# Kernel tuning notes

Measured on AMD Instinct MI355X. Metric: run time of the kernel, lower is better.

The kernel has to match this reference:

```python
import jax, jax.numpy as jnp
import numpy as np

B, L, C, K = 32, 8192, 32, 5  # batch, positions, channels(=filters), kernel_size
F = C  # residual add requires filters == input channels
BN_EPS = 1e-3      # keras BatchNormalization default epsilon
LEAKY_ALPHA = 0.3  # keras LeakyReLU default alpha


def setup_inputs() -> dict:
    key = jax.random.key(0)
    ks = jax.random.split(key, 4)
    # RandomUniform(-limit, limit) with limit = sqrt(2*3 / (2*K*F**2))
    limit = float(np.sqrt(2.0 * 3.0 / (2.0 * K * F * F)))
    return {
        "x": jax.random.normal(ks[0], (B, L, C), dtype=jnp.float32),
        # LocallyConnected 1: K unshared kernels [L, C, F], bias [L, F]
        "k1": jax.random.uniform(ks[1], (K, L, C, F), minval=-limit, maxval=limit, dtype=jnp.float32),
        "b1": jnp.zeros((L, F), dtype=jnp.float32),
        "gamma1": jnp.ones((F,), dtype=jnp.float32),
        "beta1": jnp.zeros((F,), dtype=jnp.float32),
        "mean1": jnp.zeros((F,), dtype=jnp.float32),
        "var1": jnp.ones((F,), dtype=jnp.float32),
        # LocallyConnected 2
        "k2": jax.random.uniform(ks[2], (K, L, F, F), minval=-limit, maxval=limit, dtype=jnp.float32),
        "b2": jnp.zeros((L, F), dtype=jnp.float32),
        "gamma2": jnp.ones((F,), dtype=jnp.float32),
        "beta2": jnp.zeros((F,), dtype=jnp.float32),
        "mean2": jnp.zeros((F,), dtype=jnp.float32),
        "var2": jnp.ones((F,), dtype=jnp.float32),
    }


def _locally_connected(x, kernels, bias):
    # x: [B, L, Cin]; kernels: [K, L, Cin, F]; bias: [L, F]
    # Original adds bias once inside the accumulator and once at the end -> 2*bias.
    out = 2.0 * bias
    for i in range(kernels.shape[0]):
        step = (i // 2) * (-1 if (i % 2 == 1) else 1)  # 0, 0, 1, -1, 2, -2, ...
        xs = jnp.roll(x, step, axis=1) if step != 0 else x
        out = out + jnp.einsum('blc,lcf->blf', xs, kernels[i])
    return out


def _bn(x, gamma, beta, mean, var):
    return gamma * (x - mean) * jax.lax.rsqrt(var + BN_EPS) + beta


def _leaky(x):
    return jnp.where(x >= 0, x, LEAKY_ALPHA * x)


def reference(x, k1, b1, gamma1, beta1, mean1, var1,
              k2, b2, gamma2, beta2, mean2, var2):
    h = _locally_connected(x, k1, b1)
    h = _bn(h, gamma1, beta1, mean1, var1)
    h = _leaky(h)
    h = _locally_connected(h, k2, b2)
    h = _bn(h, gamma2, beta2, mean2, var2)
    return _leaky(h + x)
```

## Files before the change

kernel.cpp:

```cpp
#include <hip/hip_runtime.h>

#define LSZ 8192
#define CCH 32
#define NL 8
#define TILE_P (NL + 3)

__global__ __launch_bounds__(512)
void lc_bn_act(const float* __restrict__ xin,
               const float* __restrict__ wgt,
               const float* __restrict__ bias,
               const float* __restrict__ gamma,
               const float* __restrict__ beta,
               const float* __restrict__ mean,
               const float* __restrict__ var,
               const float* __restrict__ xres,
               float* __restrict__ out,
               int resid)
{
    __shared__ __align__(16) float lds[TILE_P * 32 * 32];
    const int tid = threadIdx.x;
    const int l0  = blockIdx.x * NL;

    #pragma unroll
    for (int it = 0; it < (TILE_P * 1024) / 512; ++it) {
        int flat = it * 512 + tid;
        int c  = flat & 31;
        int b  = (flat >> 5) & 31;
        int tp = flat >> 10;
        int p  = (l0 + LSZ - 2 + tp) & (LSZ - 1);
        float v = xin[((size_t)b * LSZ + p) * CCH + c];
        int swz = (((b >> 2) ^ (c & 7)) << 2) | (b & 3);
        lds[tp * 1024 + c * 32 + swz] = v;
    }
    __syncthreads();

    const int wl   = tid >> 6;
    const int lane = tid & 63;
    const int fi   = lane & 7;
    const int bg   = lane >> 3;
    const int l    = l0 + wl;

    float4 acc0 = {0.f,0.f,0.f,0.f};
    float4 acc1 = {0.f,0.f,0.f,0.f};
    float4 acc2 = {0.f,0.f,0.f,0.f};
    float4 acc3 = {0.f,0.f,0.f,0.f};

    const int stepArr[5] = {0, 0, 1, -1, 2};

    #pragma unroll
    for (int i = 0; i < 5; ++i) {
        const int tp = wl + 2 - stepArr[i];
        const float* wp = wgt + (((size_t)i * LSZ + l) << 10) + (fi << 2);
        const float* xp = lds + tp * 1024;
        #pragma unroll 8
        for (int c = 0; c < 32; ++c) {
            float4 w4 = *reinterpret_cast<const float4*>(wp + (c << 5));
            float4 x4 = *reinterpret_cast<const float4*>(xp + (c << 5) + ((bg ^ (c & 7)) << 2));
            acc0.x = fmaf(x4.x, w4.x, acc0.x); acc0.y = fmaf(x4.x, w4.y, acc0.y);
            acc0.z = fmaf(x4.x, w4.z, acc0.z); acc0.w = fmaf(x4.x, w4.w, acc0.w);
            acc1.x = fmaf(x4.y, w4.x, acc1.x); acc1.y = fmaf(x4.y, w4.y, acc1.y);
            acc1.z = fmaf(x4.y, w4.z, acc1.z); acc1.w = fmaf(x4.y, w4.w, acc1.w);
            acc2.x = fmaf(x4.z, w4.x, acc2.x); acc2.y = fmaf(x4.z, w4.y, acc2.y);
            acc2.z = fmaf(x4.z, w4.z, acc2.z); acc2.w = fmaf(x4.z, w4.w, acc2.w);
            acc3.x = fmaf(x4.w, w4.x, acc3.x); acc3.y = fmaf(x4.w, w4.y, acc3.y);
            acc3.z = fmaf(x4.w, w4.z, acc3.z); acc3.w = fmaf(x4.w, w4.w, acc3.w);
        }
    }

    const int f0 = fi << 2;
    float4 g4 = *reinterpret_cast<const float4*>(gamma + f0);
    float4 t4 = *reinterpret_cast<const float4*>(beta  + f0);
    float4 m4 = *reinterpret_cast<const float4*>(mean  + f0);
    float4 v4 = *reinterpret_cast<const float4*>(var   + f0);
    float4 sc, sh;
    sc.x = g4.x * rsqrtf(v4.x + 1e-3f); sh.x = t4.x - m4.x * sc.x;
    sc.y = g4.y * rsqrtf(v4.y + 1e-3f); sh.y = t4.y - m4.y * sc.y;
    sc.z = g4.z * rsqrtf(v4.z + 1e-3f); sh.z = t4.z - m4.z * sc.z;
    sc.w = g4.w * rsqrtf(v4.w + 1e-3f); sh.w = t4.w - m4.w * sc.w;
    float4 bb = *reinterpret_cast<const float4*>(bias + l * 32 + f0);

#define EPILOG(ACC, J)                                                          \
    {                                                                           \
        int b = (bg << 2) + (J);                                                \
        size_t off = ((size_t)b * LSZ + l) * 32 + f0;                           \
        float4 t;                                                               \
        t.x = (ACC.x + 2.f * bb.x) * sc.x + sh.x;                               \
        t.y = (ACC.y + 2.f * bb.y) * sc.y + sh.y;                               \
        t.z = (ACC.z + 2.f * bb.z) * sc.z + sh.z;                               \
        t.w = (ACC.w + 2.f * bb.w) * sc.w + sh.w;                               \
        if (resid) {                                                            \
            float4 r = *reinterpret_cast<const float4*>(xres + off);            \
            t.x += r.x; t.y += r.y; t.z += r.z; t.w += r.w;                     \
        }                                                                       \
        t.x = t.x >= 0.f ? t.x : 0.3f * t.x;                                    \
        t.y = t.y >= 0.f ? t.y : 0.3f * t.y;                                    \
        t.z = t.z >= 0.f ? t.z : 0.3f * t.z;                                    \
        t.w = t.w >= 0.f ? t.w : 0.3f * t.w;                                    \
        *reinterpret_cast<float4*>(out + off) = t;                              \
    }

    EPILOG(acc0, 0)
    EPILOG(acc1, 1)
    EPILOG(acc2, 2)
    EPILOG(acc3, 3)
#undef EPILOG
}

extern "C" void kernel_launch(void* const* d_in, const int* in_sizes, int n_in,
                              void* d_out, int out_size, void* d_ws, size_t ws_size,
                              hipStream_t stream) {
    const float* x   = (const float*)d_in[0];
    const float* k1  = (const float*)d_in[1];
    const float* b1  = (const float*)d_in[2];
    const float* g1  = (const float*)d_in[3];
    const float* be1 = (const float*)d_in[4];
    const float* mn1 = (const float*)d_in[5];
    const float* vr1 = (const float*)d_in[6];
    const float* k2  = (const float*)d_in[7];
    const float* b2  = (const float*)d_in[8];
    const float* g2  = (const float*)d_in[9];
    const float* be2 = (const float*)d_in[10];
    const float* mn2 = (const float*)d_in[11];
    const float* vr2 = (const float*)d_in[12];

    float* h = (float*)d_ws;
    float* o = (float*)d_out;

    dim3 grid(LSZ / NL), block(512);
    hipLaunchKernelGGL(lc_bn_act, grid, block, 0, stream,
                       x, k1, b1, g1, be1, mn1, vr1, x, h, 0);
    hipLaunchKernelGGL(lc_bn_act, grid, block, 0, stream,
                       h, k2, b2, g2, be2, mn2, vr2, x, o, 1);
}
```

Before: 432.8 us.

## Transpose activations to position-major layout and stream weights with register prefetch

Adds a transpose kernel that rewrites x as [L][C][B]. The layer kernel then reads its shifted neighbour rows straight from global memory, with no LDS staging tile and no barrier. Weights are double-buffered in registers one 8-channel chunk ahead, blocks shrink to 256 threads with an occupancy hint, and block indices are swizzled. The first layer writes its output in the transposed layout so the second layer can consume it directly. The cost is one extra launch, one extra pass over the input, and more workspace, in exchange for cheaper loads and better latency hiding in the weight-bandwidth-bound main kernels.

```diff
diff --git a/kernel.cpp b/kernel.cpp
--- a/kernel.cpp
+++ b/kernel.cpp
@@ -1,69 +1,108 @@
 #include <hip/hip_runtime.h>
 
 #define LSZ 8192
-#define CCH 32
-#define NL 8
-#define TILE_P (NL + 3)
 
-__global__ __launch_bounds__(512)
-void lc_bn_act(const float* __restrict__ xin,
-               const float* __restrict__ wgt,
-               const float* __restrict__ bias,
-               const float* __restrict__ gamma,
-               const float* __restrict__ beta,
-               const float* __restrict__ mean,
-               const float* __restrict__ var,
-               const float* __restrict__ xres,
-               float* __restrict__ out,
-               int resid)
+__global__ __launch_bounds__(256)
+void transp_k(const float* __restrict__ x, float* __restrict__ xt)
 {
-    __shared__ __align__(16) float lds[TILE_P * 32 * 32];
-    const int tid = threadIdx.x;
-    const int l0  = blockIdx.x * NL;
+    __shared__ float lds[8454];
+    const int t    = threadIdx.x;
+    const int l0   = blockIdx.x * 8;
+    const int lane = t & 63;
 
     #pragma unroll
-    for (int it = 0; it < (TILE_P * 1024) / 512; ++it) {
-        int flat = it * 512 + tid;
-        int c  = flat & 31;
-        int b  = (flat >> 5) & 31;
-        int tp = flat >> 10;
-        int p  = (l0 + LSZ - 2 + tp) & (LSZ - 1);
-        float v = xin[((size_t)b * LSZ + p) * CCH + c];
-        int swz = (((b >> 2) ^ (c & 7)) << 2) | (b & 3);
-        lds[tp * 1024 + c * 32 + swz] = v;
+    for (int it = 0; it < 8; ++it) {
+        int b  = it * 4 + (t >> 6);
+        int l  = lane >> 3;
+        int c4 = (lane & 7) * 4;
+        float4 v = *reinterpret_cast<const float4*>(x + ((size_t)b * LSZ + l0 + l) * 32 + c4);
+        float* p = lds + l * 1057 + c4 * 33 + b;
+        p[0] = v.x; p[33] = v.y; p[66] = v.z; p[99] = v.w;
     }
     __syncthreads();
+    #pragma unroll
+    for (int it = 0; it < 8; ++it) {
+        int l  = it;
+        int c  = t >> 3;
+        int b0 = (t & 7) * 4;
+        const float* p = lds + l * 1057 + c * 33 + b0;
+        float4 v = {p[0], p[1], p[2], p[3]};
+        *reinterpret_cast<float4*>(xt + ((size_t)(l0 + l) << 10) + c * 32 + b0) = v;
+    }
+}
 
+__global__ __launch_bounds__(256, 4)
+void lc_fast(const float* __restrict__ xin_t,
+             const float* __restrict__ wgt,
+             const float* __restrict__ bias,
+             const float* __restrict__ gamma,
+             const float* __restrict__ beta,
+             const float* __restrict__ mean,
+             const float* __restrict__ var,
+             const float* __restrict__ xres,
+             float* __restrict__ out,
+             int mode)
+{
+    const int tid  = threadIdx.x;
+    const int bid  = blockIdx.x;
+    const int bs   = ((bid & 7) << 8) | (bid >> 3);
     const int wl   = tid >> 6;
     const int lane = tid & 63;
+    const int l    = (bs << 2) | wl;
     const int fi   = lane & 7;
     const int bg   = lane >> 3;
-    const int l    = l0 + wl;
 
-    float4 acc0 = {0.f,0.f,0.f,0.f};
-    float4 acc1 = {0.f,0.f,0.f,0.f};
-    float4 acc2 = {0.f,0.f,0.f,0.f};
-    float4 acc3 = {0.f,0.f,0.f,0.f};
+    const float* xr0 = xin_t + ((size_t)l << 10) + (bg << 2);
+    const float* xr2 = xin_t + ((size_t)((l - 1) & (LSZ - 1)) << 10) + (bg << 2);
+    const float* xr3 = xin_t + ((size_t)((l + 1) & (LSZ - 1)) << 10) + (bg << 2);
+    const float* xr4 = xin_t + ((size_t)((l - 2) & (LSZ - 1)) << 10) + (bg << 2);
 
-    const int stepArr[5] = {0, 0, 1, -1, 2};
+    float4 acc[4];
+    acc[0] = acc[1] = acc[2] = acc[3] = float4{0.f, 0.f, 0.f, 0.f};
+
+    const float* wbase = wgt + ((size_t)l << 10) + (fi << 2);
+
+    float4 wb[8], xb[8];
+    #pragma unroll
+    for (int u = 0; u < 8; ++u)
+        wb[u] = *reinterpret_cast<const float4*>(wbase + u * 32);
 
     #pragma unroll
-    for (int i = 0; i < 5; ++i) {
-        const int tp = wl + 2 - stepArr[i];
-        const float* wp = wgt + (((size_t)i * LSZ + l) << 10) + (fi << 2);
-        const float* xp = lds + tp * 1024;
-        #pragma unroll 8
-        for (int c = 0; c < 32; ++c) {
-            float4 w4 = *reinterpret_cast<const float4*>(wp + (c << 5));
-            float4 x4 = *reinterpret_cast<const float4*>(xp + (c << 5) + ((bg ^ (c & 7)) << 2));
-            acc0.x = fmaf(x4.x, w4.x, acc0.x); acc0.y = fmaf(x4.x, w4.y, acc0.y);
-            acc0.z = fmaf(x4.x, w4.z, acc0.z); acc0.w = fmaf(x4.x, w4.w, acc0.w);
-            acc1.x = fmaf(x4.y, w4.x, acc1.x); acc1.y = fmaf(x4.y, w4.y, acc1.y);
-            acc1.z = fmaf(x4.y, w4.z, acc1.z); acc1.w = fmaf(x4.y, w4.w, acc1.w);
-            acc2.x = fmaf(x4.z, w4.x, acc2.x); acc2.y = fmaf(x4.z, w4.y, acc2.y);
-            acc2.z = fmaf(x4.z, w4.z, acc2.z); acc2.w = fmaf(x4.z, w4.w, acc2.w);
-            acc3.x = fmaf(x4.w, w4.x, acc3.x); acc3.y = fmaf(x4.w, w4.y, acc3.y);
-            acc3.z = fmaf(x4.w, w4.z, acc3.z); acc3.w = fmaf(x4.w, w4.w, acc3.w);
+    for (int k = 0; k < 20; ++k) {
+        const int i  = k >> 2;
+        const int c0 = (k & 3) * 8;
+        const float* xrow_ = (i <= 1) ? xr0 : (i == 2 ? xr2 : (i == 3 ? xr3 : xr4));
+
+        #pragma unroll
+        for (int u = 0; u < 8; ++u)
+            xb[u] = *reinterpret_cast<const float4*>(xrow_ + (c0 + u) * 32);
+
+        float4 wn[8];
+        if (k < 19) {
+            const int kn = k + 1;
+            const float* wp_ = wbase + (size_t)(kn >> 2) * (LSZ * 1024) + ((kn & 3) * 8) * 32;
+            #pragma unroll
+            for (int u = 0; u < 8; ++u)
+                wn[u] = *reinterpret_cast<const float4*>(wp_ + u * 32);
+        }
+
+        #pragma unroll
+        for (int u = 0; u < 8; ++u) {
+            const float4 w4 = wb[u];
+            const float4 x4 = xb[u];
+            acc[0].x = fmaf(x4.x, w4.x, acc[0].x); acc[0].y = fmaf(x4.x, w4.y, acc[0].y);
+            acc[0].z = fmaf(x4.x, w4.z, acc[0].z); acc[0].w = fmaf(x4.x, w4.w, acc[0].w);
+            acc[1].x = fmaf(x4.y, w4.x, acc[1].x); acc[1].y = fmaf(x4.y, w4.y, acc[1].y);
+            acc[1].z = fmaf(x4.y, w4.z, acc[1].z); acc[1].w = fmaf(x4.y, w4.w, acc[1].w);
+            acc[2].x = fmaf(x4.z, w4.x, acc[2].x); acc[2].y = fmaf(x4.z, w4.y, acc[2].y);
+            acc[2].z = fmaf(x4.z, w4.z, acc[2].z); acc[2].w = fmaf(x4.z, w4.w, acc[2].w);
+            acc[3].x = fmaf(x4.w, w4.x, acc[3].x); acc[3].y = fmaf(x4.w, w4.y, acc[3].y);
+            acc[3].z = fmaf(x4.w, w4.z, acc[3].z); acc[3].w = fmaf(x4.w, w4.w, acc[3].w);
+        }
+
+        if (k < 19) {
+            #pragma unroll
+            for (int u = 0; u < 8; ++u) wb[u] = wn[u];
         }
     }
 
@@ -79,31 +118,48 @@
     sc.w = g4.w * rsqrtf(v4.w + 1e-3f); sh.w = t4.w - m4.w * sc.w;
     float4 bb = *reinterpret_cast<const float4*>(bias + l * 32 + f0);
 
-#define EPILOG(ACC, J)                                                          \
-    {                                                                           \
-        int b = (bg << 2) + (J);                                                \
-        size_t off = ((size_t)b * LSZ + l) * 32 + f0;                           \
-        float4 t;                                                               \
-        t.x = (ACC.x + 2.f * bb.x) * sc.x + sh.x;                               \
-        t.y = (ACC.y + 2.f * bb.y) * sc.y + sh.y;                               \
-        t.z = (ACC.z + 2.f * bb.z) * sc.z + sh.z;                               \
-        t.w = (ACC.w + 2.f * bb.w) * sc.w + sh.w;                               \
-        if (resid) {                                                            \
-            float4 r = *reinterpret_cast<const float4*>(xres + off);            \
-            t.x += r.x; t.y += r.y; t.z += r.z; t.w += r.w;                     \
-        }                                                                       \
-        t.x = t.x >= 0.f ? t.x : 0.3f * t.x;                                    \
-        t.y = t.y >= 0.f ? t.y : 0.3f * t.y;                                    \
-        t.z = t.z >= 0.f ? t.z : 0.3f * t.z;                                    \
-        t.w = t.w >= 0.f ? t.w : 0.3f * t.w;                                    \
-        *reinterpret_cast<float4*>(out + off) = t;                              \
+    if (mode == 0) {
+        float4 tb[4];
+        tb[0] = float4{acc[0].x, acc[1].x, acc[2].x, acc[3].x};
+        tb[1] = float4{acc[0].y, acc[1].y, acc[2].y, acc[3].y};
+        tb[2] = float4{acc[0].z, acc[1].z, acc[2].z, acc[3].z};
+        tb[3] = float4{acc[0].w, acc[1].w, acc[2].w, acc[3].w};
+        const float scv[4] = {sc.x, sc.y, sc.z, sc.w};
+        const float shv[4] = {sh.x, sh.y, sh.z, sh.w};
+        const float bbv[4] = {bb.x, bb.y, bb.z, bb.w};
+        #pragma unroll
+        for (int jf = 0; jf < 4; ++jf) {
+            float s_ = scv[jf], h_ = shv[jf], b_ = bbv[jf];
+            float4 t = tb[jf];
+            t.x = (t.x + 2.f * b_) * s_ + h_;
+            t.y = (t.y + 2.f * b_) * s_ + h_;
+            t.z = (t.z + 2.f * b_) * s_ + h_;
+            t.w = (t.w + 2.f * b_) * s_ + h_;
+            t.x = t.x >= 0.f ? t.x : 0.3f * t.x;
+            t.y = t.y >= 0.f ? t.y : 0.3f * t.y;
+            t.z = t.z >= 0.f ? t.z : 0.3f * t.z;
+            t.w = t.w >= 0.f ? t.w : 0.3f * t.w;
+            *reinterpret_cast<float4*>(out + ((size_t)l << 10) + (f0 + jf) * 32 + (bg << 2)) = t;
+        }
+    } else {
+        #pragma unroll
+        for (int j = 0; j < 4; ++j) {
+            int b = (bg << 2) + j;
+            size_t off = ((size_t)b * LSZ + l) * 32 + f0;
+            float4 t = acc[j];
+            t.x = (t.x + 2.f * bb.x) * sc.x + sh.x;
+            t.y = (t.y + 2.f * bb.y) * sc.y + sh.y;
+            t.z = (t.z + 2.f * bb.z) * sc.z + sh.z;
+            t.w = (t.w + 2.f * bb.w) * sc.w + sh.w;
+            float4 r = *reinterpret_cast<const float4*>(xres + off);
+            t.x += r.x; t.y += r.y; t.z += r.z; t.w += r.w;
+            t.x = t.x >= 0.f ? t.x : 0.3f * t.x;
+            t.y = t.y >= 0.f ? t.y : 0.3f * t.y;
+            t.z = t.z >= 0.f ? t.z : 0.3f * t.z;
+            t.w = t.w >= 0.f ? t.w : 0.3f * t.w;
+            *reinterpret_cast<float4*>(out + off) = t;
+        }
     }
-
-    EPILOG(acc0, 0)
-    EPILOG(acc1, 1)
-    EPILOG(acc2, 2)
-    EPILOG(acc3, 3)
-#undef EPILOG
 }
 
 extern "C" void kernel_launch(void* const* d_in, const int* in_sizes, int n_in,
@@ -123,12 +179,13 @@
     const float* mn2 = (const float*)d_in[11];
     const float* vr2 = (const float*)d_in[12];
 
-    float* h = (float*)d_ws;
-    float* o = (float*)d_out;
+    float* xt = (float*)d_ws;
+    float* ht = xt + (size_t)LSZ * 1024;
+    float* o  = (float*)d_out;
 
-    dim3 grid(LSZ / NL), block(512);
-    hipLaunchKernelGGL(lc_bn_act, grid, block, 0, stream,
-                       x, k1, b1, g1, be1, mn1, vr1, x, h, 0);
-    hipLaunchKernelGGL(lc_bn_act, grid, block, 0, stream,
-                       h, k2, b2, g2, be2, mn2, vr2, x, o, 1);
+    hipLaunchKernelGGL(transp_k, dim3(1024), dim3(256), 0, stream, x, xt);
+    hipLaunchKernelGGL(lc_fast, dim3(2048), dim3(256), 0, stream,
+                       xt, k1, b1, g1, be1, mn1, vr1, (const float*)nullptr, ht, 0);
+    hipLaunchKernelGGL(lc_fast, dim3(2048), dim3(256), 0, stream,
+                       ht, k2, b2, g2, be2, mn2, vr2, x, o, 1);
 }
```

Result: slower. 634.6 us (+46.6%).
